# Performance work log

Measured on AMD Instinct MI355X. Metric: run time of the kernel, lower is better.

The kernel has to match this reference:

```python
import jax, jax.numpy as jnp
import numpy as np


def setup_inputs() -> dict:
    key = jax.random.key(0)
    k1, k2 = jax.random.split(key)
    in_features, out_features = 4096, 4096
    tokens = 8192
    x = jax.random.normal(k1, (tokens, in_features), dtype=jnp.float32)
    # matches reset_parameters: N(0, sqrt(1/in_features))
    weight = jax.random.normal(k2, (out_features, in_features), dtype=jnp.float32) * np.sqrt(1.0 / in_features)
    bias = jnp.zeros((out_features,), dtype=jnp.float32)
    return {"x": x, "weight": weight, "bias": bias}


def reference(x, weight, bias):
    # BinaryLinearFunction.forward: binarize weight to sign(w), dense matmul, add bias
    w_bin = jnp.sign(weight)  # [out, in], values in {-1, 0, +1}
    return x @ w_bin.T + bias  # [tokens, out]
```

## Files before the change

### kernel.cpp

```cpp
#include <hip/hip_runtime.h>
#include <stdint.h>
#include <stddef.h>

typedef int i32x4 __attribute__((ext_vector_type(4)));

static constexpr int M = 8192, N = 4096, K = 4096;
static constexpr int BM = 256, BN = 256, BK = 128;
static constexpr int NT = K / BK;


__global__ __launch_bounds__(256) void quant_rows(const float* __restrict__ x,
                                                  int8_t* __restrict__ xq,
                                                  float* __restrict__ scales) {
    const int row = blockIdx.x;
    const int tid = threadIdx.x;
    const float4* xr = (const float4*)(x + (size_t)row * K);

    float4 v[4];
    float m = 0.f;
#pragma unroll
    for (int k = 0; k < 4; ++k) {
        v[k] = xr[k * 256 + tid];
        m = fmaxf(m, fmaxf(fmaxf(fabsf(v[k].x), fabsf(v[k].y)),
                           fmaxf(fabsf(v[k].z), fabsf(v[k].w))));
    }
#pragma unroll
    for (int off = 32; off; off >>= 1) m = fmaxf(m, __shfl_down(m, off, 64));

    __shared__ float wm[4];
    if ((tid & 63) == 0) wm[tid >> 6] = m;
    __syncthreads();
    const float amax = fmaxf(fmaxf(fmaxf(wm[0], wm[1]), fmaxf(wm[2], wm[3])), 1e-20f);
    const float s = 127.0f / amax;
    if (tid == 0) scales[row] = amax * (1.0f / 127.0f);

    int8_t* xo = xq + (size_t)row * K;
#pragma unroll
    for (int k = 0; k < 4; ++k) {
        int8_t o[4] = {(int8_t)__float2int_rn(v[k].x * s),
                       (int8_t)__float2int_rn(v[k].y * s),
                       (int8_t)__float2int_rn(v[k].z * s),
                       (int8_t)__float2int_rn(v[k].w * s)};
        *(int*)(xo + (k * 256 + tid) * 4) = *(const int*)o;
    }
}

__global__ __launch_bounds__(256) void binarize_w_kernel(const float* __restrict__ w,
                                                         int8_t* __restrict__ wq) {
    const size_t i = (size_t)blockIdx.x * 256 + threadIdx.x;
    float4 a = ((const float4*)w)[i];
    float vv[4] = {a.x, a.y, a.z, a.w};
    int8_t o[4];
#pragma unroll
    for (int j = 0; j < 4; ++j)
        o[j] = (vv[j] > 0.f) ? (int8_t)1 : ((vv[j] < 0.f) ? (int8_t)-1 : (int8_t)0);
    *(int*)(wq + 4 * i) = *(const int*)o;
}


__device__ __forceinline__ void async_copy16(const int8_t* g, int8_t* l) {
    __builtin_amdgcn_global_load_lds(
        (const __attribute__((address_space(1))) void*)g,
        (__attribute__((address_space(3))) void*)l,
        16, 0, 0);
}

#define SFENCE() __builtin_amdgcn_sched_barrier(0)
#define BAR() __builtin_amdgcn_s_barrier()
#define WAITVM(NN) asm volatile("s_waitcnt vmcnt(" #NN ")")

__global__ __launch_bounds__(512, 2) void gemm_i8(const int8_t* __restrict__ A,
                                                  const int8_t* __restrict__ B,
                                                  const float* __restrict__ bias,
                                                  const float* __restrict__ scales,
                                                  float* __restrict__ C) {
    __shared__ __align__(16) int8_t As[2][2][BM * 64];
    __shared__ __align__(16) int8_t Bs[2][2][BN * 64];

    const int tid  = threadIdx.x;
    const int lane = tid & 63;
    const int wave = tid >> 6;
    const int wr = wave >> 2;
    const int wc = wave & 3;
    const int q  = lane >> 4;
    const int lr = lane & 15;

    const int wg  = blockIdx.x;
    const int swz = (wg & 7) * 64 + (wg >> 3);
    const int m0  = (swz & 31) * BM;
    const int n0  = (swz >> 5) * BN;

    i32x4 acc[8][4];
#pragma unroll
    for (int mi = 0; mi < 8; ++mi)
#pragma unroll
        for (int ni = 0; ni < 4; ++ni) acc[mi][ni] = (i32x4)0;

    int aoff[8], boff[4];
#pragma unroll
    for (int mi = 0; mi < 8; ++mi) {
        const int r = wr * 128 + mi * 16 + lr;
        aoff[mi] = r * 64 + ((q ^ ((r >> 1) & 3)) * 16);
    }
#pragma unroll
    for (int ni = 0; ni < 4; ++ni) {
        const int r = wc * 64 + ni * 16 + lr;
        boff[ni] = r * 64 + ((q ^ ((r >> 1) & 3)) * 16);
    }

    const int s0 = tid, s1 = tid + 512;
    const int8_t* sA0 = A + (size_t)(m0 + (s0 >> 2)) * K + (((s0 & 3) ^ ((s0 >> 3) & 3)) * 16);
    const int8_t* sA1 = A + (size_t)(m0 + (s1 >> 2)) * K + (((s1 & 3) ^ ((s1 >> 3) & 3)) * 16);
    const int8_t* sB0 = B + (size_t)(n0 + (s0 >> 2)) * K + (((s0 & 3) ^ ((s0 >> 3) & 3)) * 16);
    const int8_t* sB1 = B + (size_t)(n0 + (s1 >> 2)) * K + (((s1 & 3) ^ ((s1 >> 3) & 3)) * 16);

#define STAGE(buf, kh, kt) do {                                    \
        const int _ko = (kt) * BK + (kh) * 64;                     \
        async_copy16(sA0 + _ko, &As[buf][kh][s0 * 16]);            \
        async_copy16(sA1 + _ko, &As[buf][kh][s1 * 16]);            \
        async_copy16(sB0 + _ko, &Bs[buf][kh][s0 * 16]);            \
        async_copy16(sB1 + _ko, &Bs[buf][kh][s1 * 16]);            \
    } while (0)

    STAGE(0, 0, 0);
    STAGE(0, 1, 0);
    STAGE(1, 0, 1);
    SFENCE();
    WAITVM(8);
    SFENCE();
    BAR();
    SFENCE();

#pragma unroll 2
    for (int t = 0; t < NT; ++t) {
        const int cur = t & 1;
        const int nxt = cur ^ 1;

        {
            const int8_t* Au = &As[cur][0][0];
            const int8_t* Bu = &Bs[cur][0][0];
            i32x4 af[8], bf[4];
#pragma unroll
            for (int mi = 0; mi < 8; ++mi) af[mi] = *(const i32x4*)(Au + aoff[mi]);
#pragma unroll
            for (int ni = 0; ni < 4; ++ni) bf[ni] = *(const i32x4*)(Bu + boff[ni]);
            if (t + 1 < NT) STAGE(nxt, 1, t + 1);
            SFENCE();
            BAR();
            SFENCE();
            __builtin_amdgcn_s_setprio(1);
#pragma unroll
            for (int mi = 0; mi < 8; ++mi)
#pragma unroll
                for (int ni = 0; ni < 4; ++ni)
                    acc[mi][ni] = __builtin_amdgcn_mfma_i32_16x16x64_i8(
                        af[mi], bf[ni], acc[mi][ni], 0, 0, 0);
            __builtin_amdgcn_s_setprio(0);
            SFENCE();
            if (t < NT - 1) { WAITVM(8); } else { WAITVM(0); }
            SFENCE();
            BAR();
            SFENCE();
        }

        {
            const int8_t* Au = &As[cur][1][0];
            const int8_t* Bu = &Bs[cur][1][0];
            i32x4 af[8], bf[4];
#pragma unroll
            for (int mi = 0; mi < 8; ++mi) af[mi] = *(const i32x4*)(Au + aoff[mi]);
#pragma unroll
            for (int ni = 0; ni < 4; ++ni) bf[ni] = *(const i32x4*)(Bu + boff[ni]);
            if (t + 2 < NT) STAGE(cur, 0, t + 2);
            SFENCE();
            BAR();
            SFENCE();
            __builtin_amdgcn_s_setprio(1);
#pragma unroll
            for (int mi = 0; mi < 8; ++mi)
#pragma unroll
                for (int ni = 0; ni < 4; ++ni)
                    acc[mi][ni] = __builtin_amdgcn_mfma_i32_16x16x64_i8(
                        af[mi], bf[ni], acc[mi][ni], 0, 0, 0);
            __builtin_amdgcn_s_setprio(0);
            SFENCE();
            if (t < NT - 2) { WAITVM(8); }
            else if (t == NT - 2) { WAITVM(4); }
            else { WAITVM(0); }
            SFENCE();
            BAR();
            SFENCE();
        }
    }
#undef STAGE

    float srow[8][4];
#pragma unroll
    for (int mi = 0; mi < 8; ++mi) {
        const int row0 = m0 + wr * 128 + mi * 16 + q * 4;
#pragma unroll
        for (int i = 0; i < 4; ++i) srow[mi][i] = scales[row0 + i];
    }
#pragma unroll
    for (int ni = 0; ni < 4; ++ni) {
        const int col = n0 + wc * 64 + ni * 16 + lr;
        const float bv = bias[col];
#pragma unroll
        for (int mi = 0; mi < 8; ++mi) {
            const int row0 = m0 + wr * 128 + mi * 16 + q * 4;
#pragma unroll
            for (int i = 0; i < 4; ++i)
                C[(size_t)(row0 + i) * N + col] = (float)acc[mi][ni][i] * srow[mi][i] + bv;
        }
    }
}


extern "C" void kernel_launch(void* const* d_in, const int* in_sizes, int n_in,
                              void* d_out, int out_size, void* d_ws, size_t ws_size,
                              hipStream_t stream) {
    const float* x    = (const float*)d_in[0];
    const float* w    = (const float*)d_in[1];
    const float* bias = (const float*)d_in[2];
    float* out        = (float*)d_out;

    float* scales = (float*)d_ws;
    int8_t* xq = (int8_t*)d_ws + 32768;
    int8_t* wq = xq + (size_t)M * K;

    quant_rows<<<M, 256, 0, stream>>>(x, xq, scales);
    binarize_w_kernel<<<(N * K / 4) / 256, 256, 0, stream>>>(w, wq);

    gemm_i8<<<dim3(512), 512, 0, stream>>>(xq, wq, bias, scales, out);
}
```

Before: 402.9 us.

## Fuse prep kernels and split GEMM k-step into A/B staged half-phases

Merges the activation quantization and weight binarization kernels into a single launch, with branching on block index, to remove one kernel launch and its tail. In the int8 GEMM main loop, each k-half now runs as two phases: first the mi 0-3 MFMAs while A is staged, then the mi 4-7 MFMAs while B is staged. Only four A fragments are held in registers at a time, which reduces VGPR pressure, and global-to-LDS copies are spread more evenly across compute. The cost is twice as many workgroup barriers per k-step, and the outer loop is no longer unrolled.

```diff
diff --git a/kernel.cpp b/kernel.cpp
--- a/kernel.cpp
+++ b/kernel.cpp
@@ -9,52 +9,54 @@
 static constexpr int NT = K / BK;
 
 
-__global__ __launch_bounds__(256) void quant_rows(const float* __restrict__ x,
-                                                  int8_t* __restrict__ xq,
-                                                  float* __restrict__ scales) {
-    const int row = blockIdx.x;
+__global__ __launch_bounds__(256) void prep(const float* __restrict__ x,
+                                            const float* __restrict__ w,
+                                            int8_t* __restrict__ xq,
+                                            float* __restrict__ scales,
+                                            int8_t* __restrict__ wq) {
+    __shared__ float wm[4];
     const int tid = threadIdx.x;
-    const float4* xr = (const float4*)(x + (size_t)row * K);
-
-    float4 v[4];
-    float m = 0.f;
-#pragma unroll
-    for (int k = 0; k < 4; ++k) {
-        v[k] = xr[k * 256 + tid];
-        m = fmaxf(m, fmaxf(fmaxf(fabsf(v[k].x), fabsf(v[k].y)),
-                           fmaxf(fabsf(v[k].z), fabsf(v[k].w))));
-    }
-#pragma unroll
-    for (int off = 32; off; off >>= 1) m = fmaxf(m, __shfl_down(m, off, 64));
-
-    __shared__ float wm[4];
-    if ((tid & 63) == 0) wm[tid >> 6] = m;
-    __syncthreads();
-    const float amax = fmaxf(fmaxf(fmaxf(wm[0], wm[1]), fmaxf(wm[2], wm[3])), 1e-20f);
-    const float s = 127.0f / amax;
-    if (tid == 0) scales[row] = amax * (1.0f / 127.0f);
-
-    int8_t* xo = xq + (size_t)row * K;
-#pragma unroll
-    for (int k = 0; k < 4; ++k) {
-        int8_t o[4] = {(int8_t)__float2int_rn(v[k].x * s),
-                       (int8_t)__float2int_rn(v[k].y * s),
-                       (int8_t)__float2int_rn(v[k].z * s),
-                       (int8_t)__float2int_rn(v[k].w * s)};
-        *(int*)(xo + (k * 256 + tid) * 4) = *(const int*)o;
-    }
-}
-
-__global__ __launch_bounds__(256) void binarize_w_kernel(const float* __restrict__ w,
-                                                         int8_t* __restrict__ wq) {
-    const size_t i = (size_t)blockIdx.x * 256 + threadIdx.x;
-    float4 a = ((const float4*)w)[i];
-    float vv[4] = {a.x, a.y, a.z, a.w};
-    int8_t o[4];
-#pragma unroll
-    for (int j = 0; j < 4; ++j)
-        o[j] = (vv[j] > 0.f) ? (int8_t)1 : ((vv[j] < 0.f) ? (int8_t)-1 : (int8_t)0);
-    *(int*)(wq + 4 * i) = *(const int*)o;
+
+    if (blockIdx.x < M) {
+        const int row = blockIdx.x;
+        const float4* xr = (const float4*)(x + (size_t)row * K);
+
+        float4 v[4];
+        float m = 0.f;
+#pragma unroll
+        for (int k = 0; k < 4; ++k) {
+            v[k] = xr[k * 256 + tid];
+            m = fmaxf(m, fmaxf(fmaxf(fabsf(v[k].x), fabsf(v[k].y)),
+                               fmaxf(fabsf(v[k].z), fabsf(v[k].w))));
+        }
+#pragma unroll
+        for (int off = 32; off; off >>= 1) m = fmaxf(m, __shfl_down(m, off, 64));
+
+        if ((tid & 63) == 0) wm[tid >> 6] = m;
+        __syncthreads();
+        const float amax = fmaxf(fmaxf(fmaxf(wm[0], wm[1]), fmaxf(wm[2], wm[3])), 1e-20f);
+        const float s = 127.0f / amax;
+        if (tid == 0) scales[row] = amax * (1.0f / 127.0f);
+
+        int8_t* xo = xq + (size_t)row * K;
+#pragma unroll
+        for (int k = 0; k < 4; ++k) {
+            int8_t o[4] = {(int8_t)__float2int_rn(v[k].x * s),
+                           (int8_t)__float2int_rn(v[k].y * s),
+                           (int8_t)__float2int_rn(v[k].z * s),
+                           (int8_t)__float2int_rn(v[k].w * s)};
+            *(int*)(xo + (k * 256 + tid) * 4) = *(const int*)o;
+        }
+    } else {
+        const size_t i = (size_t)(blockIdx.x - M) * 256 + tid;
+        float4 a = ((const float4*)w)[i];
+        float vv[4] = {a.x, a.y, a.z, a.w};
+        int8_t o[4];
+#pragma unroll
+        for (int j = 0; j < 4; ++j)
+            o[j] = (vv[j] > 0.f) ? (int8_t)1 : ((vv[j] < 0.f) ? (int8_t)-1 : (int8_t)0);
+        *(int*)(wq + 4 * i) = *(const int*)o;
+    }
 }
 
 
@@ -114,85 +116,86 @@
     const int8_t* sB0 = B + (size_t)(n0 + (s0 >> 2)) * K + (((s0 & 3) ^ ((s0 >> 3) & 3)) * 16);
     const int8_t* sB1 = B + (size_t)(n0 + (s1 >> 2)) * K + (((s1 & 3) ^ ((s1 >> 3) & 3)) * 16);
 
-#define STAGE(buf, kh, kt) do {                                    \
+#define STAGE_A(buf, kh, kt) do {                                  \
         const int _ko = (kt) * BK + (kh) * 64;                     \
         async_copy16(sA0 + _ko, &As[buf][kh][s0 * 16]);            \
         async_copy16(sA1 + _ko, &As[buf][kh][s1 * 16]);            \
+    } while (0)
+#define STAGE_B(buf, kh, kt) do {                                  \
+        const int _ko = (kt) * BK + (kh) * 64;                     \
         async_copy16(sB0 + _ko, &Bs[buf][kh][s0 * 16]);            \
         async_copy16(sB1 + _ko, &Bs[buf][kh][s1 * 16]);            \
     } while (0)
 
-    STAGE(0, 0, 0);
-    STAGE(0, 1, 0);
-    STAGE(1, 0, 1);
+    STAGE_A(0, 0, 0); STAGE_B(0, 0, 0);
+    STAGE_A(0, 1, 0); STAGE_B(0, 1, 0);
+    STAGE_A(1, 0, 1); STAGE_B(1, 0, 1);
     SFENCE();
     WAITVM(8);
     SFENCE();
     BAR();
     SFENCE();
 
-#pragma unroll 2
     for (int t = 0; t < NT; ++t) {
         const int cur = t & 1;
         const int nxt = cur ^ 1;
 
-        {
-            const int8_t* Au = &As[cur][0][0];
-            const int8_t* Bu = &Bs[cur][0][0];
-            i32x4 af[8], bf[4];
-#pragma unroll
-            for (int mi = 0; mi < 8; ++mi) af[mi] = *(const i32x4*)(Au + aoff[mi]);
+#pragma unroll
+        for (int ks = 0; ks < 2; ++ks) {
+            const int8_t* Au = &As[cur][ks][0];
+            const int8_t* Bu = &Bs[cur][ks][0];
+            i32x4 bf[4], af[4];
+
 #pragma unroll
             for (int ni = 0; ni < 4; ++ni) bf[ni] = *(const i32x4*)(Bu + boff[ni]);
-            if (t + 1 < NT) STAGE(nxt, 1, t + 1);
+#pragma unroll
+            for (int mi = 0; mi < 4; ++mi) af[mi] = *(const i32x4*)(Au + aoff[mi]);
+            if (ks == 0) { if (t + 1 < NT) STAGE_A(nxt, 1, t + 1); }
+            else         { if (t + 2 < NT) STAGE_A(cur, 0, t + 2); }
             SFENCE();
             BAR();
             SFENCE();
             __builtin_amdgcn_s_setprio(1);
 #pragma unroll
-            for (int mi = 0; mi < 8; ++mi)
+            for (int mi = 0; mi < 4; ++mi)
 #pragma unroll
                 for (int ni = 0; ni < 4; ++ni)
                     acc[mi][ni] = __builtin_amdgcn_mfma_i32_16x16x64_i8(
                         af[mi], bf[ni], acc[mi][ni], 0, 0, 0);
             __builtin_amdgcn_s_setprio(0);
             SFENCE();
-            if (t < NT - 1) { WAITVM(8); } else { WAITVM(0); }
-            SFENCE();
-            BAR();
-            SFENCE();
-        }
-
-        {
-            const int8_t* Au = &As[cur][1][0];
-            const int8_t* Bu = &Bs[cur][1][0];
-            i32x4 af[8], bf[4];
-#pragma unroll
-            for (int mi = 0; mi < 8; ++mi) af[mi] = *(const i32x4*)(Au + aoff[mi]);
-#pragma unroll
-            for (int ni = 0; ni < 4; ++ni) bf[ni] = *(const i32x4*)(Bu + boff[ni]);
-            if (t + 2 < NT) STAGE(cur, 0, t + 2);
+            BAR();
+            SFENCE();
+
+#pragma unroll
+            for (int mi = 0; mi < 4; ++mi) af[mi] = *(const i32x4*)(Au + aoff[mi + 4]);
+            if (ks == 0) { if (t + 1 < NT) STAGE_B(nxt, 1, t + 1); }
+            else         { if (t + 2 < NT) STAGE_B(cur, 0, t + 2); }
             SFENCE();
             BAR();
             SFENCE();
             __builtin_amdgcn_s_setprio(1);
 #pragma unroll
-            for (int mi = 0; mi < 8; ++mi)
+            for (int mi = 0; mi < 4; ++mi)
 #pragma unroll
                 for (int ni = 0; ni < 4; ++ni)
-                    acc[mi][ni] = __builtin_amdgcn_mfma_i32_16x16x64_i8(
-                        af[mi], bf[ni], acc[mi][ni], 0, 0, 0);
+                    acc[mi + 4][ni] = __builtin_amdgcn_mfma_i32_16x16x64_i8(
+                        af[mi], bf[ni], acc[mi + 4][ni], 0, 0, 0);
             __builtin_amdgcn_s_setprio(0);
             SFENCE();
-            if (t < NT - 2) { WAITVM(8); }
-            else if (t == NT - 2) { WAITVM(4); }
-            else { WAITVM(0); }
-            SFENCE();
-            BAR();
-            SFENCE();
-        }
-    }
-#undef STAGE
+            if (ks == 0) {
+                if (t < NT - 1) { WAITVM(8); } else { WAITVM(0); }
+            } else {
+                if (t < NT - 2) { WAITVM(8); }
+                else if (t == NT - 2) { WAITVM(4); }
+            }
+            SFENCE();
+            BAR();
+            SFENCE();
+        }
+    }
+#undef STAGE_A
+#undef STAGE_B
 
     float srow[8][4];
 #pragma unroll
@@ -228,8 +231,7 @@
     int8_t* xq = (int8_t*)d_ws + 32768;
     int8_t* wq = xq + (size_t)M * K;
 
-    quant_rows<<<M, 256, 0, stream>>>(x, xq, scales);
-    binarize_w_kernel<<<(N * K / 4) / 256, 256, 0, stream>>>(w, wq);
+    prep<<<M + (N * K / 4) / 256, 256, 0, stream>>>(x, w, xq, scales, wq);
 
     gemm_i8<<<dim3(512), 512, 0, stream>>>(xq, wq, bias, scales, out);
 }
```

Result: slower. 427.5 us (+6.1%).
